# Kernel tuning notes

Measured on AMD Instinct MI355X. Metric: run time of the kernel, lower is better.

The kernel has to match this reference:

```python
import jax, jax.numpy as jnp
import numpy as np

LEVEL_SIZES = [6, 24, 96, 384, 1536, 6144]
NUM_LABELS = sum(LEVEL_SIZES)  # 8190
IN_FEATURES = 768
BATCH = 8192


def setup_inputs() -> dict:
    key = jax.random.key(0)
    ks = jax.random.split(key, 2 * len(LEVEL_SIZES) + 1)
    inp = {"x": jax.random.normal(ks[0], (BATCH, IN_FEATURES), dtype=jnp.float32)}
    layer_in = IN_FEATURES
    for i, out in enumerate(LEVEL_SIZES):
        scale = 1.0 / np.sqrt(layer_in)
        inp[f"W{i}"] = jax.random.uniform(ks[2 * i + 1], (out, layer_in), jnp.float32, -scale, scale)
        inp[f"b{i}"] = jax.random.uniform(ks[2 * i + 2], (out,), jnp.float32, -scale, scale)
        layer_in += out
    # labels_by_level: a permutation of global label ids, split by level sizes
    rng = np.random.default_rng(42)
    inp["labels"] = jnp.asarray(rng.permutation(NUM_LABELS), dtype=jnp.int64)
    return inp


def reference(x, W0, b0, W1, b1, W2, b2, W3, b3, W4, b4, W5, b5, labels):
    Ws = [W0, W1, W2, W3, W4, W5]
    bs = [b0, b1, b2, b3, b4, b5]
    logits = jnp.zeros((x.shape[0], NUM_LABELS), dtype=x.dtype)
    cur = x
    off = 0
    for W, b, sz in zip(Ws, bs, LEVEL_SIZES):
        y = cur @ W.T + b  # [B, sz]
        lab = labels[off:off + sz]  # static slice: global columns for this level
        logits = logits.at[:, lab].set(y)
        cur = jax.nn.relu(jnp.concatenate([cur, y], axis=1))
        off += sz
    return logits
```

## Files before the change

kernel.cpp:

```cpp
#include <hip/hip_runtime.h>
#include <hip/hip_bf16.h>

#define BATCH 8192
#define NUM_LABELS 8190
#define CURW 2944
#define YW   8192

typedef __attribute__((ext_vector_type(4))) float f32x4;
typedef __attribute__((ext_vector_type(8))) short bf16x8;

#define VMCNT(n) asm volatile("s_waitcnt vmcnt(" #n ")" ::: "memory")
#define BAR() do { asm volatile("" ::: "memory"); __builtin_amdgcn_s_barrier(); asm volatile("" ::: "memory"); } while (0)
#define WAITK(n) do { asm volatile("s_waitcnt lgkmcnt(" #n ")" ::: "memory"); __builtin_amdgcn_sched_barrier(0); } while (0)

__device__ __forceinline__ unsigned short f2bf(float f) {
  unsigned u = __builtin_bit_cast(unsigned, f);
  unsigned r = u + 0x7fffu + ((u >> 16) & 1u);
  return (unsigned short)(r >> 16);
}
__device__ __forceinline__ float bf2f(unsigned short b) {
  return __builtin_bit_cast(float, (unsigned)b << 16);
}
__device__ __forceinline__ void gload_lds16(const void* g, void* l) {
  __builtin_amdgcn_global_load_lds(
      (const __attribute__((address_space(1))) void*)g,
      (__attribute__((address_space(3))) void*)l,
      16, 0, 0);
}

__global__ void k_prep_x(const float* __restrict__ x,
                         unsigned short* __restrict__ xraw,
                         unsigned short* __restrict__ cur) {
  const int TX = BATCH * 768 / 4;
  int i = blockIdx.x * 256 + threadIdx.x;
  if (i < TX) {
    float4 v = ((const float4*)x)[i];
    int e = i * 4;
    int row = e / 768;
    int col = e - row * 768;
    ushort4 a, c;
    a.x = f2bf(v.x); a.y = f2bf(v.y); a.z = f2bf(v.z); a.w = f2bf(v.w);
    c.x = f2bf(fmaxf(v.x, 0.f)); c.y = f2bf(fmaxf(v.y, 0.f));
    c.z = f2bf(fmaxf(v.z, 0.f)); c.w = f2bf(fmaxf(v.w, 0.f));
    *(ushort4*)(xraw + e) = a;
    *(ushort4*)(cur + (size_t)row * CURW + col) = c;
    return;
  }
  int j = i - TX;
  const int PP = 130;
  if (j < BATCH * PP) {
    int row = j / PP, p = j - row * PP;
    int col = p < 58 ? 774 + p : (p < 98 ? 856 + (p - 58) : 992 + (p - 98));
    cur[(size_t)row * CURW + col] = 0;
  }
}

__device__ __forceinline__ int pad2real(int kp) {
  if (kp < 774)  return kp;
  if (kp < 832)  return -1;
  if (kp < 856)  return 774 + (kp - 832);
  if (kp < 896)  return -1;
  if (kp < 992)  return 798 + (kp - 896);
  if (kp < 1024) return -1;
  if (kp < 1408) return 894 + (kp - 1024);
  return 1278 + (kp - 1408);
}

template<int KPAD, int KREAL, int NREAL>
__device__ __forceinline__ void convW(int rel, const float* __restrict__ W,
                                      unsigned short* __restrict__ Wp) {
  int n = rel / KPAD, kp = rel - n * KPAD;
  int kr = pad2real(kp);
  float v = 0.f;
  if (n < NREAL && kr >= 0) v = W[(size_t)n * KREAL + kr];
  Wp[rel] = f2bf(v);
}

__global__ void k_convert_w_all(const float* __restrict__ W0, const float* __restrict__ W1,
                                const float* __restrict__ W2, const float* __restrict__ W3,
                                const float* __restrict__ W4, const float* __restrict__ W5,
                                const int* __restrict__ labels, int* __restrict__ inv,
                                unsigned short* __restrict__ wp) {
  int i = blockIdx.x * 256 + threadIdx.x;
  if (i < NUM_LABELS) inv[labels[i]] = i;
  if (i >= 20963328) return;
  if (i < 319488) {
    if (i < 98304)       convW<768, 768, 6>  (i,          W0, wp);
    else if (i < 204800) convW<832, 774, 24> (i - 98304,  W1, wp + 98304);
    else                 convW<896, 798, 96> (i - 204800, W2, wp + 204800);
  } else {
    if (i < 712704)       convW<1024, 894, 384>  (i - 319488,  W3, wp + 319488);
    else if (i < 2875392) convW<1408, 1278, 1536>(i - 712704,  W4, wp + 712704);
    else                  convW<2944, 2814, 6144>(i - 2875392, W5, wp + 2875392);
  }
}

__global__ __launch_bounds__(256, 2) void k_fused_small(
    const unsigned short* __restrict__ xraw,
    const unsigned short* __restrict__ w0p,
    const unsigned short* __restrict__ w1p,
    const unsigned short* __restrict__ w2p,
    const float* __restrict__ b0, const float* __restrict__ b1,
    const float* __restrict__ b2,
    unsigned short* __restrict__ ybuf,
    unsigned short* __restrict__ cur) {
  __shared__ __align__(16) unsigned short As[32 * 1000];
  const int tid = threadIdx.x;
  const int l = tid & 63, w = tid >> 6;
  const int l15 = l & 15, q8 = (l >> 4) * 8;
  const int row0 = blockIdx.x * 32;
  const int mi = w >> 1;
  const int nj0 = w & 1;

  {
    const int r = tid >> 3, c8 = tid & 7;
    const unsigned short* src = xraw + (size_t)(row0 + r) * 768 + c8 * 96;
    unsigned short* dst = As + r * 1000 + c8 * 96;
#pragma unroll
    for (int i = 0; i < 12; ++i)
      *(bf16x8*)(dst + i * 8) = *(const bf16x8*)(src + i * 8);
    unsigned short* dz = As + r * 1000 + 768 + c8 * 28;
    ushort4 z = {0, 0, 0, 0};
#pragma unroll
    for (int i = 0; i < 7; ++i) *(ushort4*)(dz + i * 4) = z;
  }
  __syncthreads();

  auto level = [&](int K, int ntiles, int Nr, const unsigned short* W, int ldw,
                   const float* bias, int ycol, int ccol) {
    for (int n = nj0; n < ntiles; n += 2) {
      f32x4 acc = {0.f, 0.f, 0.f, 0.f};
      const unsigned short* wrow = W + (size_t)(n * 16 + l15) * ldw + q8;
      const unsigned short* arow = As + (mi * 16 + l15) * 1000 + q8;
#pragma unroll 2
      for (int k0 = 0; k0 < K; k0 += 32) {
        bf16x8 af = *(const bf16x8*)(arow + k0);
        bf16x8 bf = *(const bf16x8*)(wrow + k0);
        acc = __builtin_amdgcn_mfma_f32_16x16x32_bf16(af, bf, acc, 0, 0, 0);
      }
      int col = n * 16 + l15;
      if (col < Nr) {
        float bv = bias[col];
#pragma unroll
        for (int j = 0; j < 4; ++j) {
          int rl = mi * 16 + (l >> 4) * 4 + j;
          float y = acc[j] + bv;
          ybuf[(size_t)(row0 + rl) * YW + ycol + col] = f2bf(y);
          As[rl * 1000 + ccol + col] = f2bf(fmaxf(y, 0.f));
        }
      }
    }
    __syncthreads();
  };

  level(768, 1, 6,  w0p, 768, b0, 0,  768);

  {
    const int r = tid >> 3, c8 = tid & 7;
    unsigned short* p = As + r * 1000 + c8 * 96;
#pragma unroll
    for (int i = 0; i < 12; ++i) {
      bf16x8 v = *(bf16x8*)(p + i * 8);
#pragma unroll
      for (int j = 0; j < 8; ++j)
        if (((unsigned short)v[j]) & 0x8000u) v[j] = 0;
      *(bf16x8*)(p + i * 8) = v;
    }
  }
  __syncthreads();

  level(832, 2, 24, w1p, 832, b1, 6,  832);
  level(896, 6, 96, w2p, 896, b2, 30, 896);

  {
    const int r = tid >> 3, c8 = tid & 7;
    const unsigned short* srcl = As + r * 1000 + 768 + c8 * 28;
    unsigned short* dstg = cur + (size_t)(row0 + r) * CURW + 768 + c8 * 28;
#pragma unroll
    for (int i = 0; i < 7; ++i)
      *(ushort4*)(dstg + i * 4) = *(const ushort4*)(srcl + i * 4);
  }
}

__global__ __launch_bounds__(256, 2) void k_gemm(
    const unsigned short* __restrict__ A, int lda,
    const unsigned short* __restrict__ B, int ldb,
    const float* __restrict__ bias,
    unsigned short* __restrict__ ybuf,
    unsigned short* __restrict__ curout,
    int K, int Nreal, int yoff, int curoff) {
  __shared__ unsigned short Asmem[128 * 64];
  __shared__ unsigned short Bsmem[128 * 64];
  const int tid = threadIdx.x;
  const int lane = tid & 63;
  const int wid = tid >> 6;
  const int wr = wid >> 1, wc = wid & 1;
  const int brow = blockIdx.x * 128;
  const int bcol = blockIdx.y * 128;

  f32x4 acc[4][4] = {};

  for (int k0 = 0; k0 < K; k0 += 64) {
#pragma unroll
    for (int p = 0; p < 4; ++p) {
      int ch = wid * 4 + p;
      int eo = ch * 512 + lane * 8;
      int r = eo >> 6;
      int col = eo & 63;
      gload_lds16(A + (size_t)(brow + r) * lda + k0 + col, Asmem + ch * 512);
      gload_lds16(B + (size_t)(bcol + r) * ldb + k0 + col, Bsmem + ch * 512);
    }
    __syncthreads();
#pragma unroll
    for (int kk = 0; kk < 2; ++kk) {
      bf16x8 af[4], bfr[4];
      int colk = kk * 32 + (lane >> 4) * 8;
#pragma unroll
      for (int m = 0; m < 4; ++m)
        af[m] = *(const bf16x8*)(Asmem + (wr * 64 + m * 16 + (lane & 15)) * 64 + colk);
#pragma unroll
      for (int n = 0; n < 4; ++n)
        bfr[n] = *(const bf16x8*)(Bsmem + (wc * 64 + n * 16 + (lane & 15)) * 64 + colk);
#pragma unroll
      for (int m = 0; m < 4; ++m)
#pragma unroll
        for (int n = 0; n < 4; ++n)
          acc[m][n] = __builtin_amdgcn_mfma_f32_16x16x32_bf16(af[m], bfr[n], acc[m][n], 0, 0, 0);
    }
    __syncthreads();
  }

#pragma unroll
  for (int n = 0; n < 4; ++n) {
    int col = bcol + wc * 64 + n * 16 + (lane & 15);
    if (col >= Nreal) continue;
    float bv = bias[col];
#pragma unroll
    for (int m = 0; m < 4; ++m) {
#pragma unroll
      for (int j = 0; j < 4; ++j) {
        int row = brow + wr * 64 + m * 16 + (lane >> 4) * 4 + j;
        float y = acc[m][n][j] + bv;
        ybuf[(size_t)row * YW + yoff + col] = f2bf(y);
        if (curout) curout[(size_t)row * CURW + curoff + col] = f2bf(fmaxf(y, 0.f));
      }
    }
  }
}

__global__ __launch_bounds__(512, 2) void k_gemm256(
    const unsigned short* __restrict__ A, int lda,
    const unsigned short* __restrict__ B, int ldb,
    const float* __restrict__ bias,
    unsigned short* __restrict__ ybuf,
    unsigned short* __restrict__ curout,
    int K, int yoff, int curoff) {
  __shared__ __align__(16) unsigned short lds[65536];
  const int tid = threadIdx.x;
  const int l = tid & 63;
  const int w = tid >> 6;
  const int wr = w >> 2;
  const int wc = w & 3;
  const int l15 = l & 15;
  const int q8 = (l >> 4) * 8;
  const int sx = (l & 7) << 3;
  const int swz = ((l & 7) ^ (l >> 3)) * 8;

  const int bid = blockIdx.x;
  const int im = (bid & 7) * 4 + ((bid >> 3) & 3);
  const int in = bid >> 5;
  const int brow = im * 256, bcol = in * 256;

  const unsigned short* gAr0 = A + (size_t)(brow + w * 8 + (l >> 3)) * lda + swz;
  const unsigned short* gAr1 = gAr0 + (size_t)64 * lda;
  const unsigned short* gAr2 = gAr0 + (size_t)128 * lda;
  const unsigned short* gAr3 = gAr0 + (size_t)192 * lda;
  const unsigned short* gBr0 = B + (size_t)(bcol + w * 8 + (l >> 3)) * ldb + swz;
  const unsigned short* gBr1 = gBr0 + (size_t)64 * ldb;
  const unsigned short* gBr2 = gBr0 + (size_t)128 * ldb;
  const unsigned short* gBr3 = gBr0 + (size_t)192 * ldb;

  unsigned short* const dA00 = lds + w * 512;
  unsigned short* const dA01 = lds + 8192 + w * 512;
  unsigned short* const dA10 = lds + 16384 + w * 512;
  unsigned short* const dA11 = lds + 24576 + w * 512;
  unsigned short* const dB00 = lds + 32768 + w * 512;
  unsigned short* const dB01 = lds + 40960 + w * 512;
  unsigned short* const dB10 = lds + 49152 + w * 512;
  unsigned short* const dB11 = lds + 57344 + w * 512;

  const int cOff0 = (q8) ^ sx;
  const int cOff1 = (32 + q8) ^ sx;
  const int brB = (wc & 1) * 64;
  const unsigned short* const aB00 = lds + wr * 8192 + l15 * 64 + cOff0;
  const unsigned short* const aB01 = lds + wr * 8192 + l15 * 64 + cOff1;
  const unsigned short* const aB10 = lds + 16384 + wr * 8192 + l15 * 64 + cOff0;
  const unsigned short* const aB11 = lds + 16384 + wr * 8192 + l15 * 64 + cOff1;
  const unsigned short* const bB00 = lds + 32768 + (wc >> 1) * 8192 + (brB + l15) * 64 + cOff0;
  const unsigned short* const bB01 = lds + 32768 + (wc >> 1) * 8192 + (brB + l15) * 64 + cOff1;
  const unsigned short* const bB10 = lds + 49152 + (wc >> 1) * 8192 + (brB + l15) * 64 + cOff0;
  const unsigned short* const bB11 = lds + 49152 + (wc >> 1) * 8192 + (brB + l15) * 64 + cOff1;

  f32x4 acc[8][4] = {};
  bf16x8 aF[2][4], bF[2][4];

  auto stage2 = [&](const unsigned short* glo, const unsigned short* ghi,
                    unsigned short* dst, int koff) {
    gload_lds16(glo + koff, dst);
    gload_lds16(ghi + koff, dst + 4096);
  };
  auto ldAh = [&](const unsigned short* lo, const unsigned short* hi, int half) {
#pragma unroll
    for (int m = 0; m < 4; ++m) {
      aF[0][m] = *(const bf16x8*)(lo + (half * 64 + m * 16) * 64);
      aF[1][m] = *(const bf16x8*)(hi + (half * 64 + m * 16) * 64);
    }
  };
  auto ldB01f = [&](const unsigned short* lo, const unsigned short* hi) {
#pragma unroll
    for (int n = 0; n < 2; ++n) {
      bF[0][n] = *(const bf16x8*)(lo + n * 16 * 64);
      bF[1][n] = *(const bf16x8*)(hi + n * 16 * 64);
    }
  };
  auto ldB23f = [&](const unsigned short* lo, const unsigned short* hi) {
#pragma unroll
    for (int n = 2; n < 4; ++n) {
      bF[0][n] = *(const bf16x8*)(lo + n * 16 * 64);
      bF[1][n] = *(const bf16x8*)(hi + n * 16 * 64);
    }
  };
  auto MM4 = [&](int m, int mbase, int nbase) {
#pragma unroll
    for (int kk = 0; kk < 2; ++kk)
#pragma unroll
      for (int n = 0; n < 2; ++n)
        acc[mbase + m][nbase + n] = __builtin_amdgcn_mfma_f32_16x16x32_bf16(
            aF[kk][m], bF[kk][nbase + n], acc[mbase + m][nbase + n], 0, 0, 0);
  };
  auto MMAblk = [&](int mbase, int nbase) {
    __builtin_amdgcn_s_setprio(1);
#pragma unroll
    for (int kk = 0; kk < 2; ++kk)
#pragma unroll
      for (int m = 0; m < 4; ++m)
#pragma unroll
        for (int n = 0; n < 2; ++n)
          acc[mbase + m][nbase + n] = __builtin_amdgcn_mfma_f32_16x16x32_bf16(
              aF[kk][m], bF[kk][nbase + n], acc[mbase + m][nbase + n], 0, 0, 0);
    __builtin_amdgcn_s_setprio(0);
  };

#define LADDER(mb, nb, w0, w1, w2, w3) do { \
    __builtin_amdgcn_s_setprio(1); \
    WAITK(w0); MM4(0, mb, nb); \
    WAITK(w1); MM4(1, mb, nb); \
    WAITK(w2); MM4(2, mb, nb); \
    WAITK(w3); MM4(3, mb, nb); \
    __builtin_amdgcn_s_setprio(0); \
  } while (0)

  const int KT = K >> 6;
  const int NT2 = KT >> 1;

  stage2(gBr0, gBr1, dB00, 0);
  stage2(gBr2, gBr3, dB01, 0);
  stage2(gAr0, gAr1, dA00, 0);
  stage2(gAr2, gAr3, dA01, 0);
  stage2(gBr0, gBr1, dB10, 64);
  stage2(gBr2, gBr3, dB11, 64);
  stage2(gAr0, gAr1, dA10, 64);
  VMCNT(6);
  BAR();
  ldB01f(bB00, bB01);

  for (int it = 0; it < NT2; ++it) {
    const bool more = (it + 1 < NT2);
    stage2(gAr2, gAr3, dA11, 64);
    ldAh(aB00, aB01, 0);
    ldB23f(bB00, bB01);
    LADDER(0, 0, 10, 8, 6, 4);
    BAR();
    MMAblk(0, 2);
    BAR();
    if (more) stage2(gBr0, gBr1, dB00, 128);
    ldAh(aB00, aB01, 1);
    LADDER(4, 0, 6, 4, 2, 0);
    BAR();
    if (more) { stage2(gBr2, gBr3, dB01, 128); stage2(gAr0, gAr1, dA00, 128); VMCNT(6); }
    else      { VMCNT(0); }
    BAR();
    ldB01f(bB10, bB11);
    MMAblk(4, 2);
    BAR();
    if (more) stage2(gAr2, gAr3, dA01, 128);
    ldAh(aB10, aB11, 0);
    ldB23f(bB10, bB11);
    LADDER(0, 0, 10, 8, 6, 4);
    BAR();
    MMAblk(0, 2);
    BAR();
    if (more) stage2(gBr0, gBr1, dB10, 192);
    ldAh(aB10, aB11, 1);
    LADDER(4, 0, 6, 4, 2, 0);
    BAR();
    if (more) { stage2(gBr2, gBr3, dB11, 192); stage2(gAr0, gAr1, dA10, 192); VMCNT(6); }
    BAR();
    if (more) ldB01f(bB00, bB01);
    MMAblk(4, 2);
    BAR();
    gAr0 += 128; gAr1 += 128; gAr2 += 128; gAr3 += 128;
    gBr0 += 128; gBr1 += 128; gBr2 += 128; gBr3 += 128;
  }
#undef LADDER

  const int j4 = (l >> 4) * 4;
  float bv[4];
#pragma unroll
  for (int n = 0; n < 4; ++n) bv[n] = bias[bcol + wc * 64 + n * 16 + l15];
#pragma unroll
  for (int m = 0; m < 8; ++m) {
    int rowb = brow + wr * 128 + m * 16 + j4;
#pragma unroll
    for (int j = 0; j < 4; ++j) {
      size_t rbase = (size_t)(rowb + j);
#pragma unroll
      for (int n = 0; n < 4; ++n) {
        int col = bcol + wc * 64 + n * 16 + l15;
        float y = acc[m][n][j] + bv[n];
        ybuf[rbase * YW + yoff + col] = f2bf(y);
        if (curout) curout[rbase * CURW + curoff + col] = f2bf(fmaxf(y, 0.f));
      }
    }
  }
}

__global__ __launch_bounds__(256) void k_gather(
    const unsigned short* __restrict__ ybuf,
    const int* __restrict__ inv,
    float* __restrict__ out) {
  const int row = blockIdx.x;
  const unsigned short* yr = ybuf + (size_t)row * YW;
  float* orow = out + (size_t)row * NUM_LABELS;
  const int t = threadIdx.x;
#pragma unroll
  for (int it = 0; it < 16; ++it) {
    int idx = it * 256 + t;
    if (idx < NUM_LABELS / 2) {
      int c2 = idx * 2;
      int2 iv = *(const int2*)(inv + c2);
      float2 v;
      v.x = bf2f(yr[iv.x]);
      v.y = bf2f(yr[iv.y]);
      *(float2*)(orow + c2) = v;
    }
  }
}

extern "C" void kernel_launch(void* const* d_in, const int* in_sizes, int n_in,
                              void* d_out, int out_size, void* d_ws, size_t ws_size,
                              hipStream_t stream) {
  const float* x = (const float*)d_in[0];
  const float* W[6];
  const float* bias[6];
  for (int i = 0; i < 6; ++i) {
    W[i] = (const float*)d_in[1 + 2 * i];
    bias[i] = (const float*)d_in[2 + 2 * i];
  }
  const int* labels = (const int*)d_in[13];
  float* out = (float*)d_out;

  char* ws = (char*)d_ws;
  unsigned short* xraw = (unsigned short*)(ws);
  unsigned short* cur  = (unsigned short*)(ws + 12582912);
  unsigned short* wp   = (unsigned short*)(ws + 60817408);
  unsigned short* ybuf = (unsigned short*)(ws + 102744064);
  int* inv             = (int*)(ws + 236961792);

  static const int Kpad[6]   = {768, 832, 896, 1024, 1408, 2944};
  static const int Nreal[6]  = {6, 24, 96, 384, 1536, 6144};
  static const int Npad[6]   = {128, 128, 128, 384, 1536, 6144};
  static const size_t woff[6] = {0, 98304, 204800, 319488, 712704, 2875392};
  static const int yoff[6]   = {0, 6, 30, 126, 510, 2046};
  static const int curoff[6] = {768, 832, 896, 1024, 1408, 0};

  {
    int tot = BATCH * 768 / 4 + BATCH * 130;
    k_prep_x<<<(tot + 255) / 256, 256, 0, stream>>>(x, xraw, cur);
  }
  k_convert_w_all<<<(20963328 + 255) / 256, 256, 0, stream>>>(
      W[0], W[1], W[2], W[3], W[4], W[5], labels, inv, wp);

  k_fused_small<<<BATCH / 32, 256, 0, stream>>>(
      xraw, wp + woff[0], wp + woff[1], wp + woff[2],
      bias[0], bias[1], bias[2], ybuf, cur);

  {
    dim3 grid(BATCH / 128, Npad[3] / 128);
    k_gemm<<<grid, 256, 0, stream>>>(cur, CURW, wp + woff[3], Kpad[3], bias[3], ybuf,
                                     cur, Kpad[3], Nreal[3], yoff[3], curoff[3]);
  }
  for (int i = 4; i < 6; ++i) {
    int nwg = (BATCH / 256) * (Npad[i] / 256);
    k_gemm256<<<nwg, 512, 0, stream>>>(cur, CURW, wp + woff[i], Kpad[i], bias[i], ybuf,
                                       (i < 5) ? cur : (unsigned short*)nullptr,
                                       Kpad[i], yoff[i], curoff[i]);
  }

  k_gather<<<BATCH, 256, 0, stream>>>(ybuf, inv, out);
}
```

Measured before the change: 526.0 us.

## Add BK=32 double-buffered GEMM with two blocks per CU for last level

Adds a new 256x256-tile GEMM kernel with a K-step of 32 and a 64 KB double-buffered LDS ring, declared with launch bounds of (512, 2) so two workgroups can share a CU. It is used only for the largest level (6144 outputs, the dominant GEMM). The kernel staggers its MFMA issue behind partial lgkmcnt waits and raises wave priority around the MFMA block, aiming to overlap global-to-LDS loads with compute and to hide latency through the extra occupancy. The smaller K-step means twice as many barriers per K, and the occupancy bound limits the registers available to each wave.

```diff
diff --git a/kernel.cpp b/kernel.cpp
--- a/kernel.cpp
+++ b/kernel.cpp
@@ -435,6 +435,143 @@
   }
 }
 
+__global__ __launch_bounds__(512, 2) void k_gemm_bk32(
+    const unsigned short* __restrict__ A, int lda,
+    const unsigned short* __restrict__ B, int ldb,
+    const float* __restrict__ bias,
+    unsigned short* __restrict__ ybuf,
+    unsigned short* __restrict__ curout,
+    int K, int yoff, int curoff) {
+  __shared__ __align__(16) unsigned short lds[32768];
+  const int tid = threadIdx.x;
+  const int l = tid & 63;
+  const int w = tid >> 6;
+  const int wr = w >> 2;
+  const int wc = w & 3;
+  const int l15 = l & 15;
+
+  const int bid = blockIdx.x;
+  const int im = (bid & 7) * 4 + ((bid >> 3) & 3);
+  const int in = bid >> 5;
+  const int brow = im * 256, bcol = in * 256;
+
+  const int srow = w * 16 + (l >> 2);
+  const int sslot = ((l & 3) ^ ((l >> 3) & 3)) * 8;
+  const unsigned short* gA0 = A + (size_t)(brow + srow) * lda + sslot;
+  const unsigned short* gA1 = gA0 + (size_t)128 * lda;
+  const unsigned short* gB0 = B + (size_t)(bcol + srow) * ldb + sslot;
+  const unsigned short* gB1 = gB0 + (size_t)128 * ldb;
+
+  unsigned short* const sA0 = lds + w * 512;
+  unsigned short* const sA1 = lds + 8192 + w * 512;
+  unsigned short* const sB0 = lds + 16384 + w * 512;
+  unsigned short* const sB1 = lds + 24576 + w * 512;
+
+  const int rslot = (((l >> 4) ^ ((l >> 1) & 3))) * 8;
+  const unsigned short* const aR0 = lds + (wr * 128 + l15) * 32 + rslot;
+  const unsigned short* const aR1 = lds + 8192 + (wr * 128 + l15) * 32 + rslot;
+  const unsigned short* const bR0 = lds + 16384 + (wc * 64 + l15) * 32 + rslot;
+  const unsigned short* const bR1 = lds + 24576 + (wc * 64 + l15) * 32 + rslot;
+
+  f32x4 acc[8][4] = {};
+  bf16x8 aF[8], bF[4];
+
+  auto stage0 = [&](int kt) {
+    const int ko = kt * 32;
+    gload_lds16(gA0 + ko, sA0);
+    gload_lds16(gA1 + ko, sA0 + 4096);
+    gload_lds16(gB0 + ko, sB0);
+    gload_lds16(gB1 + ko, sB0 + 4096);
+  };
+  auto stage1 = [&](int kt) {
+    const int ko = kt * 32;
+    gload_lds16(gA0 + ko, sA1);
+    gload_lds16(gA1 + ko, sA1 + 4096);
+    gload_lds16(gB0 + ko, sB1);
+    gload_lds16(gB1 + ko, sB1 + 4096);
+  };
+  auto body = [&](const unsigned short* aR, const unsigned short* bR) {
+    bF[0] = *(const bf16x8*)(bR);
+    bF[1] = *(const bf16x8*)(bR + 512);
+#pragma unroll
+    for (int m = 0; m < 8; ++m)
+      aF[m] = *(const bf16x8*)(aR + m * 512);
+    bF[2] = *(const bf16x8*)(bR + 1024);
+    bF[3] = *(const bf16x8*)(bR + 1536);
+    __builtin_amdgcn_s_setprio(1);
+    WAITK(8);
+#pragma unroll
+    for (int m = 0; m < 2; ++m) {
+      acc[m][0] = __builtin_amdgcn_mfma_f32_16x16x32_bf16(aF[m], bF[0], acc[m][0], 0, 0, 0);
+      acc[m][1] = __builtin_amdgcn_mfma_f32_16x16x32_bf16(aF[m], bF[1], acc[m][1], 0, 0, 0);
+    }
+    WAITK(6);
+#pragma unroll
+    for (int m = 2; m < 4; ++m) {
+      acc[m][0] = __builtin_amdgcn_mfma_f32_16x16x32_bf16(aF[m], bF[0], acc[m][0], 0, 0, 0);
+      acc[m][1] = __builtin_amdgcn_mfma_f32_16x16x32_bf16(aF[m], bF[1], acc[m][1], 0, 0, 0);
+    }
+    WAITK(4);
+#pragma unroll
+    for (int m = 4; m < 6; ++m) {
+      acc[m][0] = __builtin_amdgcn_mfma_f32_16x16x32_bf16(aF[m], bF[0], acc[m][0], 0, 0, 0);
+      acc[m][1] = __builtin_amdgcn_mfma_f32_16x16x32_bf16(aF[m], bF[1], acc[m][1], 0, 0, 0);
+    }
+    WAITK(2);
+#pragma unroll
+    for (int m = 6; m < 8; ++m) {
+      acc[m][0] = __builtin_amdgcn_mfma_f32_16x16x32_bf16(aF[m], bF[0], acc[m][0], 0, 0, 0);
+      acc[m][1] = __builtin_amdgcn_mfma_f32_16x16x32_bf16(aF[m], bF[1], acc[m][1], 0, 0, 0);
+    }
+    WAITK(0);
+#pragma unroll
+    for (int m = 0; m < 8; ++m) {
+      acc[m][2] = __builtin_amdgcn_mfma_f32_16x16x32_bf16(aF[m], bF[2], acc[m][2], 0, 0, 0);
+      acc[m][3] = __builtin_amdgcn_mfma_f32_16x16x32_bf16(aF[m], bF[3], acc[m][3], 0, 0, 0);
+    }
+    __builtin_amdgcn_s_setprio(0);
+  };
+
+  const int KT = K >> 5;
+  const int NT2 = KT >> 1;
+
+  stage0(0);
+  VMCNT(0);
+  BAR();
+
+  for (int t = 0; t < NT2; ++t) {
+    const bool more = (t + 1 < NT2);
+    stage1(2 * t + 1);
+    body(aR0, bR0);
+    VMCNT(0);
+    BAR();
+    if (more) stage0(2 * t + 2);
+    body(aR1, bR1);
+    if (more) VMCNT(0);
+    BAR();
+  }
+
+  const int j4 = (l >> 4) * 4;
+  float bv[4];
+#pragma unroll
+  for (int n = 0; n < 4; ++n) bv[n] = bias[bcol + wc * 64 + n * 16 + l15];
+#pragma unroll
+  for (int m = 0; m < 8; ++m) {
+    int rowb = brow + wr * 128 + m * 16 + j4;
+#pragma unroll
+    for (int j = 0; j < 4; ++j) {
+      size_t rbase = (size_t)(rowb + j);
+#pragma unroll
+      for (int n = 0; n < 4; ++n) {
+        int col = bcol + wc * 64 + n * 16 + l15;
+        float y = acc[m][n][j] + bv[n];
+        ybuf[rbase * YW + yoff + col] = f2bf(y);
+        if (curout) curout[rbase * CURW + curoff + col] = f2bf(fmaxf(y, 0.f));
+      }
+    }
+  }
+}
+
 __global__ __launch_bounds__(256) void k_gather(
     const unsigned short* __restrict__ ybuf,
     const int* __restrict__ inv,
@@ -500,11 +637,16 @@
     k_gemm<<<grid, 256, 0, stream>>>(cur, CURW, wp + woff[3], Kpad[3], bias[3], ybuf,
                                      cur, Kpad[3], Nreal[3], yoff[3], curoff[3]);
   }
-  for (int i = 4; i < 6; ++i) {
-    int nwg = (BATCH / 256) * (Npad[i] / 256);
-    k_gemm256<<<nwg, 512, 0, stream>>>(cur, CURW, wp + woff[i], Kpad[i], bias[i], ybuf,
-                                       (i < 5) ? cur : (unsigned short*)nullptr,
-                                       Kpad[i], yoff[i], curoff[i]);
+  {
+    int nwg = (BATCH / 256) * (Npad[4] / 256);
+    k_gemm256<<<nwg, 512, 0, stream>>>(cur, CURW, wp + woff[4], Kpad[4], bias[4], ybuf,
+                                       cur, Kpad[4], yoff[4], curoff[4]);
+  }
+  {
+    int nwg = (BATCH / 256) * (Npad[5] / 256);
+    k_gemm_bk32<<<nwg, 512, 0, stream>>>(cur, CURW, wp + woff[5], Kpad[5], bias[5], ybuf,
+                                         (unsigned short*)nullptr,
+                                         Kpad[5], yoff[5], curoff[5]);
   }
 
   k_gather<<<BATCH, 256, 0, stream>>>(ybuf, inv, out);
```

After: 552.0 us. +5.0%, slower.
